# Kernel optimization log

Hardware: AMD Instinct MI355X
Metric: run time of the kernel (lower is better)

## Reference

```python
import jax, jax.numpy as jnp
import numpy as np

S = 28
L_COORD = 5.0
L_NOOBJ = 0.5


def _xyxy(boxes):
    # boxes [..., 4] as (cx, cy, w, h); cx,cy in grid units -> /S
    x = boxes[..., 0] / S
    y = boxes[..., 1] / S
    w = boxes[..., 2]
    h = boxes[..., 3]
    return jnp.stack([x - 0.5 * w, y - 0.5 * h, x + 0.5 * w, y + 0.5 * h], axis=-1)


def _iou_pairwise(b1, b2):
    # elementwise IoU of aligned boxes (equivalent to diag(compute_iou(...)))
    lt = jnp.maximum(b1[..., :2], b2[..., :2])
    rb = jnp.minimum(b1[..., 2:], b2[..., 2:])
    wh = jnp.maximum(rb - lt, 0.0)
    inter = wh[..., 0] * wh[..., 1]
    a1 = (b1[..., 2] - b1[..., 0]) * (b1[..., 3] - b1[..., 1])
    a2 = (b2[..., 2] - b2[..., 0]) * (b2[..., 3] - b2[..., 1])
    denom = a1 + a2 - inter
    return inter / jnp.where(denom > 0, denom, 1.0)


def setup_inputs() -> dict:
    key = jax.random.key(0)
    k1, k2, k3, k4 = jax.random.split(key, 4)
    N = 1024
    pred_tensor = jax.random.uniform(k1, (N, S, S, 30), dtype=jnp.float32)
    target_boxes = jax.random.uniform(k2, (N, S, S, 4), dtype=jnp.float32)
    target_cls = jax.random.uniform(k3, (N, S, S, 20), dtype=jnp.float32)
    has_object_map = jax.random.bernoulli(k4, 0.3, (N, S, S))
    return {"pred_tensor": pred_tensor, "target_boxes": target_boxes,
            "target_cls": target_cls, "has_object_map": has_object_map}


def reference(pred_tensor, target_boxes, target_cls, has_object_map):
    N = pred_tensor.shape[0]
    mask = has_object_map            # (N,S,S) bool
    fm = mask.astype(pred_tensor.dtype)
    pb1 = pred_tensor[..., :5]
    pb2 = pred_tensor[..., 5:10]
    pred_cls = pred_tensor[..., 10:]

    # class loss: masked sum of squared errors over object cells
    cls_loss = jnp.sum(fm[..., None] * (pred_cls - target_cls) ** 2)

    # no-object loss: confidence of both boxes on non-object cells vs 0
    nfm = 1.0 - fm
    no_obj_loss = L_NOOBJ * jnp.sum(nfm * (pb1[..., 4] ** 2 + pb2[..., 4] ** 2))

    # per-cell IoU of each predicted box vs the target box
    tgt_xyxy = _xyxy(target_boxes)
    iou1 = _iou_pairwise(_xyxy(pb1[..., :4]), tgt_xyxy)
    iou2 = _iou_pairwise(_xyxy(pb2[..., :4]), tgt_xyxy)
    take1 = iou1 > iou2
    best_iou = jnp.where(take1, iou1, iou2)           # (N,S,S)
    best_box = jnp.where(take1[..., None], pb1, pb2)  # (N,S,S,5)

    xy_loss = jnp.sum(fm[..., None] * (best_box[..., :2] - target_boxes[..., :2]) ** 2)
    wh_p = jnp.sqrt(jnp.where(mask[..., None], best_box[..., 2:4], 1.0))
    wh_t = jnp.sqrt(jnp.where(mask[..., None], target_boxes[..., 2:4], 1.0))
    wh_loss = jnp.sum(fm[..., None] * (wh_p - wh_t) ** 2)
    reg_loss = L_COORD * (xy_loss + wh_loss)

    # containing-object confidence loss; target IoU is detached
    contain_obj_loss = jnp.sum(fm * (best_box[..., 4] - jax.lax.stop_gradient(best_iou)) ** 2)

    total_loss = cls_loss + no_obj_loss + contain_obj_loss + reg_loss
    return jnp.stack([total_loss, reg_loss, contain_obj_loss, no_obj_loss, cls_loss]) / N
```

## Files before the change

### kernel.cpp

```cpp
#include <hip/hip_runtime.h>


#define SS 28
#define BLOCK 256

__global__ __launch_bounds__(BLOCK) void yolo_main(
    const float* __restrict__ pred,
    const float4* __restrict__ tbox4,
    const float4* __restrict__ tcls4,
    const int*   __restrict__ mask,
    float4* __restrict__ block_part,
    int cells)
{
    int cell = blockIdx.x * BLOCK + threadIdx.x;

    float acc_cls = 0.f, acc_noobj = 0.f, acc_reg = 0.f, acc_cont = 0.f;

    if (cell < cells) {
        bool m = mask[cell] != 0;
        const float* pc = pred + (size_t)cell * 30;

        if (!m) {
            float c1 = pc[4];
            float c2 = pc[9];
            acc_noobj = c1 * c1 + c2 * c2;
        } else {
            float pr[30];
            const float2* p2 = (const float2*)pc;
            #pragma unroll
            for (int i = 0; i < 15; ++i) {
                float2 v = p2[i];
                pr[2 * i] = v.x; pr[2 * i + 1] = v.y;
            }
            float4 tb = tbox4[cell];

            {
                const float4* t4 = tcls4 + (size_t)cell * 5;
                float cls = 0.f;
                #pragma unroll
                for (int i = 0; i < 5; ++i) {
                    float4 v = t4[i];
                    float d0 = pr[10 + 4 * i + 0] - v.x;
                    float d1 = pr[10 + 4 * i + 1] - v.y;
                    float d2 = pr[10 + 4 * i + 2] - v.z;
                    float d3 = pr[10 + 4 * i + 3] - v.w;
                    cls += d0 * d0 + d1 * d1 + d2 * d2 + d3 * d3;
                }
                acc_cls = cls;
            }

            const float invS = 1.f / 28.f;
            float txc = tb.x * invS, tyc = tb.y * invS;
            float t0 = txc - 0.5f * tb.z, t1 = tyc - 0.5f * tb.w;
            float t2 = txc + 0.5f * tb.z, t3 = tyc + 0.5f * tb.w;
            float ta = (t2 - t0) * (t3 - t1);

            float b1xc = pr[0] * invS, b1yc = pr[1] * invS;
            float a0 = b1xc - 0.5f * pr[2], a1 = b1yc - 0.5f * pr[3];
            float a2 = b1xc + 0.5f * pr[2], a3 = b1yc + 0.5f * pr[3];
            float wx = fmaxf(fminf(a2, t2) - fmaxf(a0, t0), 0.f);
            float wy = fmaxf(fminf(a3, t3) - fmaxf(a1, t1), 0.f);
            float inter = wx * wy;
            float area1 = (a2 - a0) * (a3 - a1);
            float den = area1 + ta - inter;
            float iou1 = inter / (den > 0.f ? den : 1.f);

            float b2xc = pr[5] * invS, b2yc = pr[6] * invS;
            float c0 = b2xc - 0.5f * pr[7], c1 = b2yc - 0.5f * pr[8];
            float c2 = b2xc + 0.5f * pr[7], c3 = b2yc + 0.5f * pr[8];
            wx = fmaxf(fminf(c2, t2) - fmaxf(c0, t0), 0.f);
            wy = fmaxf(fminf(c3, t3) - fmaxf(c1, t1), 0.f);
            inter = wx * wy;
            float area2 = (c2 - c0) * (c3 - c1);
            den = area2 + ta - inter;
            float iou2 = inter / (den > 0.f ? den : 1.f);

            bool take1 = iou1 > iou2;
            float best_iou = take1 ? iou1 : iou2;
            float bbx = take1 ? pr[0] : pr[5];
            float bby = take1 ? pr[1] : pr[6];
            float bbw = take1 ? pr[2] : pr[7];
            float bbh = take1 ? pr[3] : pr[8];
            float bbc = take1 ? pr[4] : pr[9];

            float dx = bbx - tb.x, dy = bby - tb.y;
            float xy = dx * dx + dy * dy;

            float dw = sqrtf(bbw) - sqrtf(tb.z);
            float dh = sqrtf(bbh) - sqrtf(tb.w);
            float wh = dw * dw + dh * dh;

            acc_reg = xy + wh;

            float dc = bbc - best_iou;
            acc_cont = dc * dc;
        }
    }

    float4 v = make_float4(acc_cls, acc_noobj, acc_reg, acc_cont);
    #pragma unroll
    for (int off = 32; off >= 1; off >>= 1) {
        v.x += __shfl_down(v.x, off, 64);
        v.y += __shfl_down(v.y, off, 64);
        v.z += __shfl_down(v.z, off, 64);
        v.w += __shfl_down(v.w, off, 64);
    }
    __shared__ float4 sred[BLOCK / 64];
    int lane = threadIdx.x & 63;
    int wave = threadIdx.x >> 6;
    if (lane == 0) sred[wave] = v;
    __syncthreads();
    if (threadIdx.x == 0) {
        float4 r = sred[0];
        #pragma unroll
        for (int w = 1; w < BLOCK / 64; ++w) {
            r.x += sred[w].x; r.y += sred[w].y; r.z += sred[w].z; r.w += sred[w].w;
        }
        block_part[blockIdx.x] = r;
    }
}

__global__ __launch_bounds__(BLOCK) void yolo_final(
    const float4* __restrict__ part, int nparts, float* __restrict__ out, float invN)
{
    float4 v = make_float4(0.f, 0.f, 0.f, 0.f);
    for (int i = threadIdx.x; i < nparts; i += BLOCK) {
        float4 p = part[i];
        v.x += p.x; v.y += p.y; v.z += p.z; v.w += p.w;
    }
    #pragma unroll
    for (int off = 32; off >= 1; off >>= 1) {
        v.x += __shfl_down(v.x, off, 64);
        v.y += __shfl_down(v.y, off, 64);
        v.z += __shfl_down(v.z, off, 64);
        v.w += __shfl_down(v.w, off, 64);
    }
    __shared__ float4 sred[BLOCK / 64];
    int lane = threadIdx.x & 63;
    int wave = threadIdx.x >> 6;
    if (lane == 0) sred[wave] = v;
    __syncthreads();
    if (threadIdx.x == 0) {
        float4 r = sred[0];
        #pragma unroll
        for (int w = 1; w < BLOCK / 64; ++w) {
            r.x += sred[w].x; r.y += sred[w].y; r.z += sred[w].z; r.w += sred[w].w;
        }
        float cls    = r.x;
        float no_obj = 0.5f * r.y;
        float reg    = 5.0f * r.z;
        float cont   = r.w;
        float total  = cls + no_obj + cont + reg;
        out[0] = total  * invN;
        out[1] = reg    * invN;
        out[2] = cont   * invN;
        out[3] = no_obj * invN;
        out[4] = cls    * invN;
    }
}

extern "C" void kernel_launch(void* const* d_in, const int* in_sizes, int n_in,
                              void* d_out, int out_size, void* d_ws, size_t ws_size,
                              hipStream_t stream) {
    const float* pred = (const float*)d_in[0];
    const float* tbox = (const float*)d_in[1];
    const float* tcls = (const float*)d_in[2];
    const int*   mask = (const int*)d_in[3];
    float* out = (float*)d_out;

    int cells = in_sizes[0] / 30;
    int n_img = cells / (SS * SS);
    int nblocks = (cells + BLOCK - 1) / BLOCK;

    float4* part = (float4*)d_ws;

    yolo_main<<<nblocks, BLOCK, 0, stream>>>(
        pred, (const float4*)tbox, (const float4*)tcls, mask, part, cells);
    yolo_final<<<1, BLOCK, 0, stream>>>(part, nblocks, out, 1.0f / (float)n_img);
}
```

Measured before the change: 200.0 us.

## Stage predictions through LDS with coalesced float4 loads and cooperative class loss

Each block now loads its tile of prediction rows into shared memory using coalesced float4 reads, skipping float4 chunks that only hold class data of non-object cells. The per-cell box math then reads from LDS, and the class loss is computed cooperatively: threads walk the target-class float4 array in order so those global reads are coalesced. The aim is to replace the earlier strided per-thread 120-byte row reads, which coalesce poorly, with contiguous access. The cost is about 30KB of LDS per block, which may reduce occupancy, plus extra barriers and integer division for chunk indexing.

```diff
diff --git a/kernel.cpp b/kernel.cpp
--- a/kernel.cpp
+++ b/kernel.cpp
@@ -3,51 +3,64 @@
 
 #define SS 28
 #define BLOCK 256
+#define TILE 256
+#define NP4 (TILE * 30 / 4)
+#define NT4 (TILE * 5)
 
 __global__ __launch_bounds__(BLOCK) void yolo_main(
-    const float* __restrict__ pred,
+    const float4* __restrict__ pred4,
     const float4* __restrict__ tbox4,
     const float4* __restrict__ tcls4,
     const int*   __restrict__ mask,
     float4* __restrict__ block_part,
     int cells)
 {
-    int cell = blockIdx.x * BLOCK + threadIdx.x;
+    __shared__ float spred[TILE * 30];
+    __shared__ int   smask[TILE];
+    __shared__ float4 sred[BLOCK / 64];
+
+    const int tid   = threadIdx.x;
+    const int tile0 = blockIdx.x * TILE;
+    const int tcells = min(TILE, cells - tile0);
+
+    if (tid < tcells) smask[tid] = mask[tile0 + tid];
+    else              smask[tid] = 0;
+    __syncthreads();
+
+    {
+        const size_t base4 = (size_t)tile0 * 30 / 4;
+        const size_t lim4  = (size_t)cells * 30 / 4;
+        #pragma unroll
+        for (int it = 0; it < (NP4 + BLOCK - 1) / BLOCK; ++it) {
+            int p = tid + it * BLOCK;
+            if (p >= NP4) break;
+            int f0 = 4 * p;
+            int c0 = f0 / 30;
+            int c3 = (f0 + 3) / 30;
+            bool need = (smask[c0] | smask[c3]) != 0;
+            if (!need) {
+                int comp0 = f0 - c0 * 30;
+                need = (comp0 >= 1 && comp0 <= 4) || (comp0 >= 6 && comp0 <= 9);
+            }
+            if (need && (base4 + p) < lim4) {
+                float4 v = pred4[base4 + p];
+                spred[f0 + 0] = v.x; spred[f0 + 1] = v.y;
+                spred[f0 + 2] = v.z; spred[f0 + 3] = v.w;
+            }
+        }
+    }
+    __syncthreads();
 
     float acc_cls = 0.f, acc_noobj = 0.f, acc_reg = 0.f, acc_cont = 0.f;
 
-    if (cell < cells) {
-        bool m = mask[cell] != 0;
-        const float* pc = pred + (size_t)cell * 30;
-
+    if (tid < tcells) {
+        const float* pr = spred + tid * 30;
+        bool m = smask[tid] != 0;
         if (!m) {
-            float c1 = pc[4];
-            float c2 = pc[9];
+            float c1 = pr[4], c2 = pr[9];
             acc_noobj = c1 * c1 + c2 * c2;
         } else {
-            float pr[30];
-            const float2* p2 = (const float2*)pc;
-            #pragma unroll
-            for (int i = 0; i < 15; ++i) {
-                float2 v = p2[i];
-                pr[2 * i] = v.x; pr[2 * i + 1] = v.y;
-            }
-            float4 tb = tbox4[cell];
-
-            {
-                const float4* t4 = tcls4 + (size_t)cell * 5;
-                float cls = 0.f;
-                #pragma unroll
-                for (int i = 0; i < 5; ++i) {
-                    float4 v = t4[i];
-                    float d0 = pr[10 + 4 * i + 0] - v.x;
-                    float d1 = pr[10 + 4 * i + 1] - v.y;
-                    float d2 = pr[10 + 4 * i + 2] - v.z;
-                    float d3 = pr[10 + 4 * i + 3] - v.w;
-                    cls += d0 * d0 + d1 * d1 + d2 * d2 + d3 * d3;
-                }
-                acc_cls = cls;
-            }
+            float4 tb = tbox4[tile0 + tid];
 
             const float invS = 1.f / 28.f;
             float txc = tb.x * invS, tyc = tb.y * invS;
@@ -97,6 +110,23 @@
         }
     }
 
+    {
+        const size_t tbase4 = (size_t)tile0 * 5;
+        #pragma unroll
+        for (int it = 0; it < NT4 / BLOCK; ++it) {
+            int q  = tid + it * BLOCK;
+            int cl = q / 5;
+            if (cl < tcells && smask[cl]) {
+                float4 t = tcls4[tbase4 + q];
+                int comp = q - cl * 5;
+                const float* pp = spred + cl * 30 + 10 + comp * 4;
+                float d0 = pp[0] - t.x, d1 = pp[1] - t.y;
+                float d2 = pp[2] - t.z, d3 = pp[3] - t.w;
+                acc_cls += d0 * d0 + d1 * d1 + d2 * d2 + d3 * d3;
+            }
+        }
+    }
+
     float4 v = make_float4(acc_cls, acc_noobj, acc_reg, acc_cont);
     #pragma unroll
     for (int off = 32; off >= 1; off >>= 1) {
@@ -105,7 +135,6 @@
         v.z += __shfl_down(v.z, off, 64);
         v.w += __shfl_down(v.w, off, 64);
     }
-    __shared__ float4 sred[BLOCK / 64];
     int lane = threadIdx.x & 63;
     int wave = threadIdx.x >> 6;
     if (lane == 0) sred[wave] = v;
@@ -170,11 +199,12 @@
 
     int cells = in_sizes[0] / 30;
     int n_img = cells / (SS * SS);
-    int nblocks = (cells + BLOCK - 1) / BLOCK;
+    int nblocks = (cells + TILE - 1) / TILE;
 
     float4* part = (float4*)d_ws;
 
     yolo_main<<<nblocks, BLOCK, 0, stream>>>(
-        pred, (const float4*)tbox, (const float4*)tcls, mask, part, cells);
+        (const float4*)pred, (const float4*)tbox, (const float4*)tcls,
+        mask, part, cells);
     yolo_final<<<1, BLOCK, 0, stream>>>(part, nblocks, out, 1.0f / (float)n_img);
 }
```

Result: slower. 205.3 us (+2.7%).

## Stage predictions through LDS with wave-coalesced, mask-selective float4 loads

Applied to the files above, without the earlier changes.

Each wavefront now loads its 64 cells' prediction rows cooperatively as contiguous float4 loads into shared memory, replacing the strided per-thread float2 loads. Each lane uses the mask, fetched via shuffles, to skip float4 chunks that hold only class or box data for non-object cells. Target class vectors are also loaded coalesced across the wave and only for object cells, with the class-loss terms spread across lanes. The aim is better memory coalescing and fewer bytes fetched. The cost is about 30KB of LDS per block, which can limit occupancy, plus extra index arithmetic, and the code relies on wave-level LDS visibility without a barrier.

```diff
diff --git a/kernel.cpp b/kernel.cpp
--- a/kernel.cpp
+++ b/kernel.cpp
@@ -3,52 +3,84 @@
 
 #define SS 28
 #define BLOCK 256
+#define WAVES (BLOCK / 64)
 
 __global__ __launch_bounds__(BLOCK) void yolo_main(
-    const float* __restrict__ pred,
+    const float4* __restrict__ pred4,
     const float4* __restrict__ tbox4,
     const float4* __restrict__ tcls4,
     const int*   __restrict__ mask,
     float4* __restrict__ block_part,
     int cells)
 {
-    int cell = blockIdx.x * BLOCK + threadIdx.x;
+    __shared__ float  spred[WAVES][64 * 30];
+    __shared__ float4 sred[WAVES];
+
+    const int tid    = threadIdx.x;
+    const int lane   = tid & 63;
+    const int wid    = tid >> 6;
+    const int wcell0 = blockIdx.x * BLOCK + wid * 64;
+    const int cell   = wcell0 + lane;
+
+    int m = 0;
+    if (cell < cells) m = mask[cell];
+
+    float4 tb = make_float4(0.f, 0.f, 0.f, 0.f);
+    if (m) tb = tbox4[cell];
+
+    const size_t lim4 = (size_t)cells * 30 / 4;
+    const size_t pb4  = (size_t)wcell0 * 30 / 4;
+    float4 v[8];
+    bool   nd[8];
+    int    fo[8];
+    #pragma unroll
+    for (int it = 0; it < 8; ++it) {
+        int p  = it * 64 + lane;
+        int f0 = 4 * p;
+        int c0 = f0 / 30;
+        int c3 = (f0 + 3) / 30;
+        int r0 = f0 - 30 * c0;
+        int cc0 = c0 > 63 ? 63 : c0;
+        int cc3 = c3 > 63 ? 63 : c3;
+        int m0 = __shfl(m, cc0, 64);
+        int m3 = __shfl(m, cc3, 64);
+        bool need = (p < 480) && (pb4 + (size_t)p < lim4) &&
+                    ((m0 | m3) || (r0 >= 1 && r0 <= 4) || (r0 >= 6 && r0 <= 9));
+        nd[it] = need;
+        fo[it] = f0;
+        if (need) v[it] = pred4[pb4 + p];
+    }
+
+    const size_t tb4 = (size_t)wcell0 * 5;
+    float4 t[5];
+    bool   tn[5];
+    int    tc[5], tk[5];
+    #pragma unroll
+    for (int it = 0; it < 5; ++it) {
+        int q = it * 64 + lane;
+        int c = q / 5;
+        int mc = __shfl(m, c, 64);
+        tn[it] = mc != 0;
+        tc[it] = c;
+        tk[it] = q - 5 * c;
+        if (mc) t[it] = tcls4[tb4 + q];
+    }
+
+    float* sp = spred[wid];
+    #pragma unroll
+    for (int it = 0; it < 8; ++it) {
+        if (nd[it]) *(float4*)(sp + fo[it]) = v[it];
+    }
+    asm volatile("s_waitcnt lgkmcnt(0)" ::: "memory");
 
     float acc_cls = 0.f, acc_noobj = 0.f, acc_reg = 0.f, acc_cont = 0.f;
 
     if (cell < cells) {
-        bool m = mask[cell] != 0;
-        const float* pc = pred + (size_t)cell * 30;
-
+        const float* pr = sp + lane * 30;
         if (!m) {
-            float c1 = pc[4];
-            float c2 = pc[9];
+            float c1 = pr[4], c2 = pr[9];
             acc_noobj = c1 * c1 + c2 * c2;
         } else {
-            float pr[30];
-            const float2* p2 = (const float2*)pc;
-            #pragma unroll
-            for (int i = 0; i < 15; ++i) {
-                float2 v = p2[i];
-                pr[2 * i] = v.x; pr[2 * i + 1] = v.y;
-            }
-            float4 tb = tbox4[cell];
-
-            {
-                const float4* t4 = tcls4 + (size_t)cell * 5;
-                float cls = 0.f;
-                #pragma unroll
-                for (int i = 0; i < 5; ++i) {
-                    float4 v = t4[i];
-                    float d0 = pr[10 + 4 * i + 0] - v.x;
-                    float d1 = pr[10 + 4 * i + 1] - v.y;
-                    float d2 = pr[10 + 4 * i + 2] - v.z;
-                    float d3 = pr[10 + 4 * i + 3] - v.w;
-                    cls += d0 * d0 + d1 * d1 + d2 * d2 + d3 * d3;
-                }
-                acc_cls = cls;
-            }
-
             const float invS = 1.f / 28.f;
             float txc = tb.x * invS, tyc = tb.y * invS;
             float t0 = txc - 0.5f * tb.z, t1 = tyc - 0.5f * tb.w;
@@ -97,7 +129,45 @@
         }
     }
 
-    float4 v = make_float4(acc_cls, acc_noobj, acc_reg, acc_cont);
+    #pragma unroll
+    for (int it = 0; it < 5; ++it) {
+        if (tn[it]) {
+            const float* pp = sp + tc[it] * 30 + 10 + 4 * tk[it];
+            float4 tt = t[it];
+            float d0 = pp[0] - tt.x, d1 = pp[1] - tt.y;
+            float d2 = pp[2] - tt.z, d3 = pp[3] - tt.w;
+            acc_cls += d0 * d0 + d1 * d1 + d2 * d2 + d3 * d3;
+        }
+    }
+
+    float4 vr = make_float4(acc_cls, acc_noobj, acc_reg, acc_cont);
+    #pragma unroll
+    for (int off = 32; off >= 1; off >>= 1) {
+        vr.x += __shfl_down(vr.x, off, 64);
+        vr.y += __shfl_down(vr.y, off, 64);
+        vr.z += __shfl_down(vr.z, off, 64);
+        vr.w += __shfl_down(vr.w, off, 64);
+    }
+    if (lane == 0) sred[wid] = vr;
+    __syncthreads();
+    if (tid == 0) {
+        float4 r = sred[0];
+        #pragma unroll
+        for (int w = 1; w < WAVES; ++w) {
+            r.x += sred[w].x; r.y += sred[w].y; r.z += sred[w].z; r.w += sred[w].w;
+        }
+        block_part[blockIdx.x] = r;
+    }
+}
+
+__global__ __launch_bounds__(BLOCK) void yolo_final(
+    const float4* __restrict__ part, int nparts, float* __restrict__ out, float invN)
+{
+    float4 v = make_float4(0.f, 0.f, 0.f, 0.f);
+    for (int i = threadIdx.x; i < nparts; i += BLOCK) {
+        float4 p = part[i];
+        v.x += p.x; v.y += p.y; v.z += p.z; v.w += p.w;
+    }
     #pragma unroll
     for (int off = 32; off >= 1; off >>= 1) {
         v.x += __shfl_down(v.x, off, 64);
@@ -116,36 +186,6 @@
         for (int w = 1; w < BLOCK / 64; ++w) {
             r.x += sred[w].x; r.y += sred[w].y; r.z += sred[w].z; r.w += sred[w].w;
         }
-        block_part[blockIdx.x] = r;
-    }
-}
-
-__global__ __launch_bounds__(BLOCK) void yolo_final(
-    const float4* __restrict__ part, int nparts, float* __restrict__ out, float invN)
-{
-    float4 v = make_float4(0.f, 0.f, 0.f, 0.f);
-    for (int i = threadIdx.x; i < nparts; i += BLOCK) {
-        float4 p = part[i];
-        v.x += p.x; v.y += p.y; v.z += p.z; v.w += p.w;
-    }
-    #pragma unroll
-    for (int off = 32; off >= 1; off >>= 1) {
-        v.x += __shfl_down(v.x, off, 64);
-        v.y += __shfl_down(v.y, off, 64);
-        v.z += __shfl_down(v.z, off, 64);
-        v.w += __shfl_down(v.w, off, 64);
-    }
-    __shared__ float4 sred[BLOCK / 64];
-    int lane = threadIdx.x & 63;
-    int wave = threadIdx.x >> 6;
-    if (lane == 0) sred[wave] = v;
-    __syncthreads();
-    if (threadIdx.x == 0) {
-        float4 r = sred[0];
-        #pragma unroll
-        for (int w = 1; w < BLOCK / 64; ++w) {
-            r.x += sred[w].x; r.y += sred[w].y; r.z += sred[w].z; r.w += sred[w].w;
-        }
         float cls    = r.x;
         float no_obj = 0.5f * r.y;
         float reg    = 5.0f * r.z;
@@ -175,6 +215,7 @@
     float4* part = (float4*)d_ws;
 
     yolo_main<<<nblocks, BLOCK, 0, stream>>>(
-        pred, (const float4*)tbox, (const float4*)tcls, mask, part, cells);
+        (const float4*)pred, (const float4*)tbox, (const float4*)tcls,
+        mask, part, cells);
     yolo_final<<<1, BLOCK, 0, stream>>>(part, nblocks, out, 1.0f / (float)n_img);
 }
```

New measurement: 236.5 us. 1.18x slower.

## Stage tiles into LDS with async global_load_lds double buffering per wave

Applied to the files above, without the earlier changes.

Each 64-thread block now handles four 64-cell tiles. Their pred, target box, target class and mask data are staged into a double-buffered LDS region with the asynchronous global_load_lds builtin, and explicit vmcnt waits overlap the next tile's loads with the current tile's compute. The loads are fully coalesced float4 streams instead of per-thread strided 120-byte rows. The class loss is now spread across all lanes through the float4 layout, with each lane checking the owning cell's mask. It relies on cells being divisible by 256 (no tail handling), on hand-written waitcnt counts being right, and on getting less occupancy from the larger LDS footprint per block. It also loads all class data even for masked-out cells, which the old code skipped.

```diff
diff --git a/kernel.cpp b/kernel.cpp
--- a/kernel.cpp
+++ b/kernel.cpp
@@ -2,102 +2,167 @@
 
 
 #define SS 28
-#define BLOCK 256
+#define BLOCK 64
+
+#define P_OFF  0
+#define TB_OFF 1920
+#define TC_OFF 2176
+#define MK_OFF 3456
+#define BUFSZ  3520
+
+typedef const __attribute__((address_space(1))) void* as1cp;
+typedef __attribute__((address_space(3))) void* as3p;
 
 __global__ __launch_bounds__(BLOCK) void yolo_main(
-    const float* __restrict__ pred,
+    const float4* __restrict__ pred4,
     const float4* __restrict__ tbox4,
     const float4* __restrict__ tcls4,
     const int*   __restrict__ mask,
     float4* __restrict__ block_part,
     int cells)
 {
-    int cell = blockIdx.x * BLOCK + threadIdx.x;
+    __shared__ float lds[2 * BUFSZ];
+
+    const int lane = threadIdx.x & 63;
+    const int t0   = blockIdx.x * 4;
 
     float acc_cls = 0.f, acc_noobj = 0.f, acc_reg = 0.f, acc_cont = 0.f;
 
-    if (cell < cells) {
-        bool m = mask[cell] != 0;
-        const float* pc = pred + (size_t)cell * 30;
-
-        if (!m) {
-            float c1 = pc[4];
-            float c2 = pc[9];
-            acc_noobj = c1 * c1 + c2 * c2;
-        } else {
-            float pr[30];
-            const float2* p2 = (const float2*)pc;
-            #pragma unroll
-            for (int i = 0; i < 15; ++i) {
-                float2 v = p2[i];
-                pr[2 * i] = v.x; pr[2 * i + 1] = v.y;
-            }
-            float4 tb = tbox4[cell];
-
-            {
-                const float4* t4 = tcls4 + (size_t)cell * 5;
-                float cls = 0.f;
-                #pragma unroll
-                for (int i = 0; i < 5; ++i) {
-                    float4 v = t4[i];
-                    float d0 = pr[10 + 4 * i + 0] - v.x;
-                    float d1 = pr[10 + 4 * i + 1] - v.y;
-                    float d2 = pr[10 + 4 * i + 2] - v.z;
-                    float d3 = pr[10 + 4 * i + 3] - v.w;
-                    cls += d0 * d0 + d1 * d1 + d2 * d2 + d3 * d3;
-                }
-                acc_cls = cls;
-            }
-
-            const float invS = 1.f / 28.f;
-            float txc = tb.x * invS, tyc = tb.y * invS;
-            float t0 = txc - 0.5f * tb.z, t1 = tyc - 0.5f * tb.w;
-            float t2 = txc + 0.5f * tb.z, t3 = tyc + 0.5f * tb.w;
-            float ta = (t2 - t0) * (t3 - t1);
-
-            float b1xc = pr[0] * invS, b1yc = pr[1] * invS;
-            float a0 = b1xc - 0.5f * pr[2], a1 = b1yc - 0.5f * pr[3];
-            float a2 = b1xc + 0.5f * pr[2], a3 = b1yc + 0.5f * pr[3];
-            float wx = fmaxf(fminf(a2, t2) - fmaxf(a0, t0), 0.f);
-            float wy = fmaxf(fminf(a3, t3) - fmaxf(a1, t1), 0.f);
-            float inter = wx * wy;
-            float area1 = (a2 - a0) * (a3 - a1);
-            float den = area1 + ta - inter;
-            float iou1 = inter / (den > 0.f ? den : 1.f);
-
-            float b2xc = pr[5] * invS, b2yc = pr[6] * invS;
-            float c0 = b2xc - 0.5f * pr[7], c1 = b2yc - 0.5f * pr[8];
-            float c2 = b2xc + 0.5f * pr[7], c3 = b2yc + 0.5f * pr[8];
-            wx = fmaxf(fminf(c2, t2) - fmaxf(c0, t0), 0.f);
-            wy = fmaxf(fminf(c3, t3) - fmaxf(c1, t1), 0.f);
-            inter = wx * wy;
-            float area2 = (c2 - c0) * (c3 - c1);
-            den = area2 + ta - inter;
-            float iou2 = inter / (den > 0.f ? den : 1.f);
-
-            bool take1 = iou1 > iou2;
-            float best_iou = take1 ? iou1 : iou2;
-            float bbx = take1 ? pr[0] : pr[5];
-            float bby = take1 ? pr[1] : pr[6];
-            float bbw = take1 ? pr[2] : pr[7];
-            float bbh = take1 ? pr[3] : pr[8];
-            float bbc = take1 ? pr[4] : pr[9];
-
-            float dx = bbx - tb.x, dy = bby - tb.y;
-            float xy = dx * dx + dy * dy;
-
-            float dw = sqrtf(bbw) - sqrtf(tb.z);
-            float dh = sqrtf(bbh) - sqrtf(tb.w);
-            float wh = dw * dw + dh * dh;
-
-            acc_reg = xy + wh;
-
-            float dc = bbc - best_iou;
-            acc_cont = dc * dc;
-        }
-    }
-
-    float4 v = make_float4(acc_cls, acc_noobj, acc_reg, acc_cont);
+#define ISSUE(T, BUF)                                                        \
+    {                                                                        \
+        float* bp = lds + (BUF) * BUFSZ;                                     \
+        const size_t pb4 = (size_t)(T) * 480;                                \
+        _Pragma("unroll")                                                    \
+        for (int it = 0; it < 8; ++it) {                                     \
+            int p = it * 64 + lane;                                          \
+            if (p < 480)        \
+                __builtin_amdgcn_global_load_lds(                            \
+                    (as1cp)(pred4 + pb4 + p),                                \
+                    (as3p)(bp + P_OFF + it * 256), 16, 0, 0);                \
+        }                                                                    \
+        __builtin_amdgcn_global_load_lds(                                    \
+            (as1cp)(tbox4 + (size_t)(T) * 64 + lane),                        \
+            (as3p)(bp + TB_OFF), 16, 0, 0);                                  \
+        _Pragma("unroll")                                                    \
+        for (int it = 0; it < 5; ++it)                                       \
+            __builtin_amdgcn_global_load_lds(                                \
+                (as1cp)(tcls4 + (size_t)(T) * 320 + it * 64 + lane),         \
+                (as3p)(bp + TC_OFF + it * 256), 16, 0, 0);                   \
+        __builtin_amdgcn_global_load_lds(                                    \
+            (as1cp)(mask + (size_t)(T) * 64 + lane),                         \
+            (as3p)(bp + MK_OFF), 4, 0, 0);                                   \
+    }
+
+#define WAITV(N)                                                             \
+    asm volatile("s_waitcnt vmcnt(" #N ")" ::: "memory");                    \
+    __builtin_amdgcn_sched_barrier(0);
+
+#define LGKM0 asm volatile("s_waitcnt lgkmcnt(0)" ::: "memory");
+
+#define COMPUTE(BUF)                                                         \
+    {                                                                        \
+        const float* bp = lds + (BUF) * BUFSZ;                               \
+        const int*  mi = (const int*)(bp + MK_OFF);                          \
+        int m = mi[lane];                                                    \
+        const float* pr = bp + P_OFF + lane * 30;                            \
+        if (!m) {                                                            \
+            float c1 = pr[4], c2 = pr[9];                                    \
+            acc_noobj += c1 * c1 + c2 * c2;                                  \
+        } else {                                                             \
+            const float4 tb = ((const float4*)(bp + TB_OFF))[lane];          \
+            const float invS = 1.f / 28.f;                                   \
+            float txc = tb.x * invS, tyc = tb.y * invS;                      \
+            float t0_ = txc - 0.5f * tb.z, t1_ = tyc - 0.5f * tb.w;          \
+            float t2_ = txc + 0.5f * tb.z, t3_ = tyc + 0.5f * tb.w;          \
+            float ta = (t2_ - t0_) * (t3_ - t1_);                            \
+            float b1xc = pr[0] * invS, b1yc = pr[1] * invS;                  \
+            float a0 = b1xc - 0.5f * pr[2], a1 = b1yc - 0.5f * pr[3];        \
+            float a2 = b1xc + 0.5f * pr[2], a3 = b1yc + 0.5f * pr[3];        \
+            float wx = fmaxf(fminf(a2, t2_) - fmaxf(a0, t0_), 0.f);          \
+            float wy = fmaxf(fminf(a3, t3_) - fmaxf(a1, t1_), 0.f);          \
+            float inter = wx * wy;                                           \
+            float area1 = (a2 - a0) * (a3 - a1);                             \
+            float den = area1 + ta - inter;                                  \
+            float iou1 = inter / (den > 0.f ? den : 1.f);                    \
+            float b2xc = pr[5] * invS, b2yc = pr[6] * invS;                  \
+            float e0 = b2xc - 0.5f * pr[7], e1 = b2yc - 0.5f * pr[8];        \
+            float e2 = b2xc + 0.5f * pr[7], e3 = b2yc + 0.5f * pr[8];        \
+            wx = fmaxf(fminf(e2, t2_) - fmaxf(e0, t0_), 0.f);                \
+            wy = fmaxf(fminf(e3, t3_) - fmaxf(e1, t1_), 0.f);                \
+            inter = wx * wy;                                                 \
+            float area2 = (e2 - e0) * (e3 - e1);                             \
+            den = area2 + ta - inter;                                        \
+            float iou2 = inter / (den > 0.f ? den : 1.f);                    \
+            bool take1 = iou1 > iou2;                                        \
+            float best_iou = take1 ? iou1 : iou2;                            \
+            float bbx = take1 ? pr[0] : pr[5];                               \
+            float bby = take1 ? pr[1] : pr[6];                               \
+            float bbw = take1 ? pr[2] : pr[7];                               \
+            float bbh = take1 ? pr[3] : pr[8];                               \
+            float bbc = take1 ? pr[4] : pr[9];                               \
+            float dx = bbx - tb.x, dy = bby - tb.y;                          \
+            float xy = dx * dx + dy * dy;                                    \
+            float dw = sqrtf(bbw) - sqrtf(tb.z);                             \
+            float dh = sqrtf(bbh) - sqrtf(tb.w);                             \
+            float wh = dw * dw + dh * dh;                                    \
+            acc_reg += xy + wh;                                              \
+            float dc = bbc - best_iou;                                       \
+            acc_cont += dc * dc;                                             \
+        }                                                                    \
+        _Pragma("unroll")                                                    \
+        for (int it = 0; it < 5; ++it) {                                     \
+            int q = it * 64 + lane;                                          \
+            int c = q / 5;                                                   \
+            int k = q - 5 * c;                                               \
+            if (mi[c]) {                                                     \
+                const float4 tt = ((const float4*)(bp + TC_OFF))[q];         \
+                const float* pp = bp + P_OFF + c * 30 + 10 + 4 * k;          \
+                float d0 = pp[0] - tt.x, d1 = pp[1] - tt.y;                  \
+                float d2 = pp[2] - tt.z, d3 = pp[3] - tt.w;                  \
+                acc_cls += d0 * d0 + d1 * d1 + d2 * d2 + d3 * d3;            \
+            }                                                                \
+        }                                                                    \
+    }
+
+    ISSUE(t0 + 0, 0)
+    ISSUE(t0 + 1, 1)
+    WAITV(15)
+    COMPUTE(0)
+    LGKM0
+    ISSUE(t0 + 2, 0)
+    WAITV(15)
+    COMPUTE(1)
+    LGKM0
+    ISSUE(t0 + 3, 1)
+    WAITV(15)
+    COMPUTE(0)
+    WAITV(0)
+    COMPUTE(1)
+
+#undef ISSUE
+#undef WAITV
+#undef LGKM0
+#undef COMPUTE
+
+    float4 vr = make_float4(acc_cls, acc_noobj, acc_reg, acc_cont);
+    #pragma unroll
+    for (int off = 32; off >= 1; off >>= 1) {
+        vr.x += __shfl_down(vr.x, off, 64);
+        vr.y += __shfl_down(vr.y, off, 64);
+        vr.z += __shfl_down(vr.z, off, 64);
+        vr.w += __shfl_down(vr.w, off, 64);
+    }
+    if (lane == 0) block_part[blockIdx.x] = vr;
+}
+
+__global__ __launch_bounds__(256) void yolo_final(
+    const float4* __restrict__ part, int nparts, float* __restrict__ out, float invN)
+{
+    float4 v = make_float4(0.f, 0.f, 0.f, 0.f);
+    for (int i = threadIdx.x; i < nparts; i += 256) {
+        float4 p = part[i];
+        v.x += p.x; v.y += p.y; v.z += p.z; v.w += p.w;
+    }
     #pragma unroll
     for (int off = 32; off >= 1; off >>= 1) {
         v.x += __shfl_down(v.x, off, 64);
@@ -105,7 +170,7 @@
         v.z += __shfl_down(v.z, off, 64);
         v.w += __shfl_down(v.w, off, 64);
     }
-    __shared__ float4 sred[BLOCK / 64];
+    __shared__ float4 sred[4];
     int lane = threadIdx.x & 63;
     int wave = threadIdx.x >> 6;
     if (lane == 0) sred[wave] = v;
@@ -113,37 +178,7 @@
     if (threadIdx.x == 0) {
         float4 r = sred[0];
         #pragma unroll
-        for (int w = 1; w < BLOCK / 64; ++w) {
-            r.x += sred[w].x; r.y += sred[w].y; r.z += sred[w].z; r.w += sred[w].w;
-        }
-        block_part[blockIdx.x] = r;
-    }
-}
-
-__global__ __launch_bounds__(BLOCK) void yolo_final(
-    const float4* __restrict__ part, int nparts, float* __restrict__ out, float invN)
-{
-    float4 v = make_float4(0.f, 0.f, 0.f, 0.f);
-    for (int i = threadIdx.x; i < nparts; i += BLOCK) {
-        float4 p = part[i];
-        v.x += p.x; v.y += p.y; v.z += p.z; v.w += p.w;
-    }
-    #pragma unroll
-    for (int off = 32; off >= 1; off >>= 1) {
-        v.x += __shfl_down(v.x, off, 64);
-        v.y += __shfl_down(v.y, off, 64);
-        v.z += __shfl_down(v.z, off, 64);
-        v.w += __shfl_down(v.w, off, 64);
-    }
-    __shared__ float4 sred[BLOCK / 64];
-    int lane = threadIdx.x & 63;
-    int wave = threadIdx.x >> 6;
-    if (lane == 0) sred[wave] = v;
-    __syncthreads();
-    if (threadIdx.x == 0) {
-        float4 r = sred[0];
-        #pragma unroll
-        for (int w = 1; w < BLOCK / 64; ++w) {
+        for (int w = 1; w < 4; ++w) {
             r.x += sred[w].x; r.y += sred[w].y; r.z += sred[w].z; r.w += sred[w].w;
         }
         float cls    = r.x;
@@ -170,11 +205,12 @@
 
     int cells = in_sizes[0] / 30;
     int n_img = cells / (SS * SS);
-    int nblocks = (cells + BLOCK - 1) / BLOCK;
+    int nblocks = cells / 256;
 
     float4* part = (float4*)d_ws;
 
     yolo_main<<<nblocks, BLOCK, 0, stream>>>(
-        pred, (const float4*)tbox, (const float4*)tcls, mask, part, cells);
-    yolo_final<<<1, BLOCK, 0, stream>>>(part, nblocks, out, 1.0f / (float)n_img);
+        (const float4*)pred, (const float4*)tbox, (const float4*)tcls,
+        mask, part, cells);
+    yolo_final<<<1, 256, 0, stream>>>(part, nblocks, out, 1.0f / (float)n_img);
 }
```

Result: slower. 211.7 us (+5.9%).
